# Kernel tuning notes

Hardware: AMD Instinct MI355X
Metric: run time of the kernel (lower is better)

The kernel has to match this reference:

```python
import jax, jax.numpy as jnp
from jax import lax
import numpy as np

T, B, D, H = 2048, 32, 256, 256

def setup_inputs() -> dict:
    key = jax.random.key(0)
    ks = jax.random.split(key, 8)
    inp = {
        'input_': jax.random.normal(ks[0], (T, B, D), dtype=jnp.float32),
        'length': jax.random.randint(ks[1], (B,), 0, T, dtype=jnp.int64),
        'Wih0': jax.random.normal(ks[2], (D, 3 * H), dtype=jnp.float32) * 0.05,
        'Whh0': jax.random.normal(ks[3], (H, 3 * H), dtype=jnp.float32) * 0.05,
        'b0': jax.random.normal(ks[4], (3 * H,), dtype=jnp.float32) * 0.05,
        'Wih1': jax.random.normal(ks[5], (H, 3 * H), dtype=jnp.float32) * 0.05,
        'Whh1': jax.random.normal(ks[6], (H, 3 * H), dtype=jnp.float32) * 0.05,
        'b1': jax.random.normal(ks[7], (3 * H,), dtype=jnp.float32) * 0.05,
    }
    return inp


def _run_layer(x, length, Wih, Whh, b, h0):
    # x: [T, B, D_in]; scan over time with hidden state carried on-chip.
    def step(h, xs):
        x_t, t_idx = xs
        pre = h @ Whh + x_t @ Wih + b          # [B, 3H]
        h_pre, t_pre, _c_pre = jnp.split(pre, 3, axis=1)
        t_gate = jax.nn.sigmoid(t_pre)
        c_gate = jax.nn.sigmoid(t_gate)         # bug-faithful: sigmoid of sigmoid(t_pre)
        s_t = jnp.tanh(h_pre) * t_gate + h * c_gate
        mask = (t_idx < length)[:, None]         # [B, 1]
        h_next = jnp.where(mask, s_t, h)
        return h_next, h_next
    times = jnp.arange(x.shape[0])
    h_n, out = lax.scan(step, h0, (x, times))
    return out, h_n


def reference(input_, length, Wih0, Whh0, b0, Wih1, Whh1, b1):
    h0 = jnp.zeros((input_.shape[1], H), dtype=input_.dtype)
    out0, hn0 = _run_layer(input_, length, Wih0, Whh0, b0, h0)
    # dropout=0 -> identity between layers; each layer reuses the same zero h_0
    out1, hn1 = _run_layer(out0, length, Wih1, Whh1, b1, h0)
    h_n = jnp.stack([hn0, hn1], axis=0)          # [num_layers, B, H]
    return out1, h_n
```

## Files before the change

kernel.cpp:

```cpp
#include <hip/hip_runtime.h>
#include <cstdint>
#include <cstddef>

static constexpr int T_STEPS = 2048;
static constexpr int BATCH   = 32;
static constexpr int DIM     = 256;
static constexpr int NCOL    = 512;
static constexpr size_t M_ROWS = (size_t)T_STEPS * BATCH;

typedef _Float16 f16x4 __attribute__((ext_vector_type(4)));
typedef _Float16 f16x8 __attribute__((ext_vector_type(8)));
typedef float    f32x4 __attribute__((ext_vector_type(4)));
struct alignas(8) H4 { _Float16 x, y, z, w; };

static constexpr size_t XW_OFF   = 0;
static constexpr size_t A_OFF    = M_ROWS * NCOL * 2;
static constexpr size_t BLOB_OFF = A_OFF + M_ROWS * DIM * 2;
static constexpr size_t BLOB_ELT = (size_t)DIM * NCOL;
static constexpr size_t FLAG_OFF = BLOB_OFF + 4 * BLOB_ELT * 2;

__global__ void cvt_f32_to_f16(const float* __restrict__ src, _Float16* __restrict__ dst,
                               int n4, int* __restrict__ flags) {
  if (blockIdx.x == 0 && threadIdx.x < BATCH) flags[threadIdx.x] = 0;
  int i = blockIdx.x * blockDim.x + threadIdx.x;
  if (i >= n4) return;
  float4 v = ((const float4*)src)[i];
  H4 o; o.x = (_Float16)v.x; o.y = (_Float16)v.y; o.z = (_Float16)v.z; o.w = (_Float16)v.w;
  ((H4*)dst)[i] = o;
}

__global__ void prep_blobs4(const float* __restrict__ w0, const float* __restrict__ w1,
                            const float* __restrict__ w2, const float* __restrict__ w3,
                            _Float16* __restrict__ blobs) {
  int gid = blockIdx.x * blockDim.x + threadIdx.x;
  int mat = gid >> 17;
  int rem = gid & 131071;
  int k = rem >> 9;
  int n = rem & 511;
  const float* src = (mat == 0) ? w0 : (mat == 1) ? w1 : (mat == 2) ? w2 : w3;
  float v = src[k * 768 + n];
  int kc = k >> 5, q = (k >> 3) & 3, j = k & 7, tn = n >> 4;
  int lane = (n & 15) + 16 * q;
  blobs[(size_t)mat * BLOB_ELT + ((size_t)(tn * 8 + kc) * 64 + lane) * 8 + j] = (_Float16)v;
}

__global__ __launch_bounds__(256) void gemm_xw(const _Float16* __restrict__ A,
                                               const _Float16* __restrict__ blob,
                                               const float* __restrict__ bias,
                                               _Float16* __restrict__ XW) {
  int lane = threadIdx.x & 63;
  int wave = threadIdx.x >> 6;
  int wid  = blockIdx.x * 4 + wave;
  int mbase = (wid >> 1) * 16;
  int nhalf = wid & 1;
  int q = lane >> 4, n15 = lane & 15;

  f32x4 acc[16];
#pragma unroll
  for (int i = 0; i < 16; i++) acc[i] = (f32x4){0.f, 0.f, 0.f, 0.f};

  const _Float16* Arow = A + (size_t)(mbase + n15) * DIM + q * 8;
#pragma unroll
  for (int kc = 0; kc < 8; kc++) {
    f16x8 af = *(const f16x8*)(Arow + kc * 32);
#pragma unroll
    for (int nt = 0; nt < 16; nt++) {
      const _Float16* bp = blob + ((size_t)((nhalf * 16 + nt) * 8 + kc) * 64 + lane) * 8;
      f16x8 bf = *(const f16x8*)bp;
      acc[nt] = __builtin_amdgcn_mfma_f32_16x16x32_f16(af, bf, acc[nt], 0, 0, 0);
    }
  }
#pragma unroll
  for (int nt = 0; nt < 16; nt++) {
    int col = nhalf * 256 + nt * 16 + n15;
    float bv = bias[col];
#pragma unroll
    for (int r = 0; r < 4; r++) {
      int m = mbase + q * 4 + r;
      XW[(size_t)m * NCOL + col] = (_Float16)(acc[nt][r] + bv);
    }
  }
}

__device__ __forceinline__ int read_len(const void* p, int b) {
  const long long* q = (const long long*)p;
  bool ok64 = true;
  for (int i = 0; i < 32; i++) { long long v = q[i]; if (v < 0 || v > 2048) ok64 = false; }
  return ok64 ? (int)q[b] : ((const int*)p)[b];
}

__device__ __forceinline__ void gload_lds_row(const _Float16* g, _Float16* l) {
  __builtin_amdgcn_global_load_lds(
      (const __attribute__((address_space(1))) void*)g,
      (__attribute__((address_space(3))) void*)l, 16, 0, 0);
}

__device__ __forceinline__ void gate_update(float pre_h, float pre_t, bool live, float& h) {
  const float K1 = 1.442695040888963f, K2 = 2.885390081777927f;
  float phc = fminf(fmaxf(pre_h, -20.f), 20.f);
  float e1 = __builtin_amdgcn_exp2f(-K2 * phc);
  float e2 = __builtin_amdgcn_exp2f(-K1 * pre_t);
  float u1 = 1.f + e1;
  float rr = __builtin_amdgcn_rcpf(u1 * (1.f + e2));
  float ttg = (1.f - e1) * rr;
  float tg  = u1 * rr;
  float cg = 0.5f + tg * (0.250905f + tg * (-0.00432f + tg * (-0.015525f)));
  float s = ttg + h * cg;
  h = live ? s : h;
}

__global__ __launch_bounds__(512, 2) void recur_fused(const _Float16* __restrict__ xw0,
                                                      const _Float16* __restrict__ bwhh0,
                                                      const _Float16* __restrict__ bwhh1,
                                                      const _Float16* __restrict__ bwih1,
                                                      const float* __restrict__ b1,
                                                      const void* __restrict__ lenp,
                                                      _Float16* __restrict__ out0,
                                                      float* __restrict__ out1,
                                                      float* __restrict__ hn,
                                                      int* __restrict__ flags) {
  const int bid  = blockIdx.x;
  const int tid  = threadIdx.x;
  const int w    = tid >> 6;
  const int lane = tid & 63;
  const int q = lane >> 4, l15 = lane & 15;

  __shared__ __align__(16) _Float16 hbuf[2][DIM];
  __shared__ __align__(16) _Float16 xbuf[2][16][NCOL];

  const int c0 = (2 * w) * 16 + l15;
  const int c1 = (2 * w + 1) * 16 + l15;
  constexpr int NB = T_STEPS / 16;

  if (bid < BATCH) {
    const int b = bid;
    const int len = read_len(lenp, b);
    f16x8 Bh[2][8], Bt[2][8];
#pragma unroll
    for (int pp = 0; pp < 2; pp++)
#pragma unroll
      for (int kc = 0; kc < 8; kc++) {
        Bh[pp][kc] = *(const f16x8*)(bwhh0 + ((size_t)((2 * w + pp) * 8 + kc) * 64 + lane) * 8);
        Bt[pp][kc] = *(const f16x8*)(bwhh0 + ((size_t)((16 + 2 * w + pp) * 8 + kc) * 64 + lane) * 8);
      }
    if (tid < DIM) hbuf[0][tid] = (_Float16)0.f;

    const _Float16* xrow = xw0 + (size_t)b * NCOL;
    const size_t xstride = (size_t)BATCH * NCOL;

    gload_lds_row(xrow + (size_t)(2 * w)     * xstride + lane * 8, &xbuf[0][2 * w][0]);
    gload_lds_row(xrow + (size_t)(2 * w + 1) * xstride + lane * 8, &xbuf[0][2 * w + 1][0]);
    asm volatile("s_waitcnt vmcnt(0)" ::: "memory");
    __syncthreads();

    float h0 = 0.f, h1 = 0.f;
    for (int tb = 0; tb < NB; ++tb) {
      const int buf = tb & 1;
      if (tb + 1 < NB) {
        const _Float16* gsrc = xrow + (size_t)((tb + 1) * 16) * xstride;
        gload_lds_row(gsrc + (size_t)(2 * w)     * xstride + lane * 8, &xbuf[1 - buf][2 * w][0]);
        gload_lds_row(gsrc + (size_t)(2 * w + 1) * xstride + lane * 8, &xbuf[1 - buf][2 * w + 1][0]);
      }
#pragma unroll
      for (int ts = 0; ts < 16; ++ts) {
        const int t = tb * 16 + ts;
        const int p = ts & 1;
        const _Float16* xr = &xbuf[buf][ts][0];
        const float xh0 = (float)xr[c0],       xh1 = (float)xr[c1];
        const float xt0 = (float)xr[c0 + 256], xt1 = (float)xr[c1 + 256];

        f32x4 a0 = {0.f, 0.f, 0.f, 0.f}, a1 = a0, a2 = a0, a3 = a0;
        const _Float16* hb = &hbuf[p][q * 8];
#pragma unroll
        for (int kc = 0; kc < 8; kc++) {
          f16x8 a = *(const f16x8*)(hb + kc * 32);
          a0 = __builtin_amdgcn_mfma_f32_16x16x32_f16(a, Bh[0][kc], a0, 0, 0, 0);
          a1 = __builtin_amdgcn_mfma_f32_16x16x32_f16(a, Bh[1][kc], a1, 0, 0, 0);
          a2 = __builtin_amdgcn_mfma_f32_16x16x32_f16(a, Bt[0][kc], a2, 0, 0, 0);
          a3 = __builtin_amdgcn_mfma_f32_16x16x32_f16(a, Bt[1][kc], a3, 0, 0, 0);
        }
        const bool live = t < len;
        gate_update(a0[0] + xh0, a2[0] + xt0, live, h0);
        gate_update(a1[0] + xh1, a3[0] + xt1, live, h1);
        _Float16 s0 = (_Float16)h0, s1 = (_Float16)h1;
        if (q == 0) {
          hbuf[1 - p][c0] = s0;
          hbuf[1 - p][c1] = s1;
          size_t o = ((size_t)t * BATCH + b) * DIM;
          out0[o + c0] = s0; out0[o + c1] = s1;
        }
        if (ts == 15) {
          asm volatile("s_waitcnt vmcnt(0) lgkmcnt(0)\n\ts_barrier" ::: "memory");
        } else {
          asm volatile("s_waitcnt lgkmcnt(0)\n\ts_barrier" ::: "memory");
        }
      }
      if (tid == 0)
        __hip_atomic_store(&flags[b], tb + 1, __ATOMIC_RELEASE, __HIP_MEMORY_SCOPE_AGENT);
    }
    if (q == 0) {
      hn[b * DIM + c0] = h0;
      hn[b * DIM + c1] = h1;
    }
  } else {
    const int b = bid - BATCH;
    const int len = read_len(lenp, b);
    f16x8 Bh[2][8], Bt[2][8];
#pragma unroll
    for (int pp = 0; pp < 2; pp++)
#pragma unroll
      for (int kc = 0; kc < 8; kc++) {
        Bh[pp][kc] = *(const f16x8*)(bwhh1 + ((size_t)((2 * w + pp) * 8 + kc) * 64 + lane) * 8);
        Bt[pp][kc] = *(const f16x8*)(bwhh1 + ((size_t)((16 + 2 * w + pp) * 8 + kc) * 64 + lane) * 8);
      }
    const float bb0 = b1[c0], bb1 = b1[c1], bb2 = b1[c0 + 256], bb3 = b1[c1 + 256];
    if (tid < DIM) hbuf[0][tid] = (_Float16)0.f;
    __syncthreads();

#define WAIT_FLAG(TH_)                                                                   \
    {                                                                                    \
      int it = 0;                                                                        \
      while (__hip_atomic_load(&flags[b], __ATOMIC_RELAXED, __HIP_MEMORY_SCOPE_AGENT)    \
             < (TH_)) {                                                                  \
        __builtin_amdgcn_s_sleep(2);                                                     \
        if (++it > (1 << 22)) break;           \
      }                                                                                  \
      (void)__hip_atomic_load(&flags[b], __ATOMIC_ACQUIRE, __HIP_MEMORY_SCOPE_AGENT);    \
    }

#define XGEMM(XA_, DST_)                                                                 \
    {                                                                                    \
      _Pragma("unroll")                                                                  \
      for (int ti = 0; ti < 4; ti++) {                                                   \
        const int tn = (ti < 2) ? (2 * w + ti) : (16 + 2 * w + (ti - 2));                \
        f32x4 acc = {0.f, 0.f, 0.f, 0.f};                                                \
        _Pragma("unroll")                                                                \
        for (int kc = 0; kc < 8; kc++) {                                                 \
          f16x8 bf = *(const f16x8*)(bwih1 + ((size_t)(tn * 8 + kc) * 64 + lane) * 8);   \
          acc = __builtin_amdgcn_mfma_f32_16x16x32_f16(XA_[kc], bf, acc, 0, 0, 0);       \
        }                                                                                \
        const int   col = (ti == 0) ? c0 : (ti == 1) ? c1 : (ti == 2) ? (c0 + 256)       \
                                                                      : (c1 + 256);      \
        const float bv  = (ti == 0) ? bb0 : (ti == 1) ? bb1 : (ti == 2) ? bb2 : bb3;     \
        _Pragma("unroll")                                                                \
        for (int r = 0; r < 4; r++) xbuf[DST_][q * 4 + r][col] = (_Float16)(acc[r] + bv);\
      }                                                                                  \
    }

    float h0 = 0.f, h1 = 0.f;

    WAIT_FLAG(1);
    {
      const _Float16* arow = out0 + ((size_t)l15 * BATCH + b) * DIM + q * 8;
      f16x8 xa0[8];
#pragma unroll
      for (int kc = 0; kc < 8; kc++) xa0[kc] = *(const f16x8*)(arow + kc * 32);
      XGEMM(xa0, 0);
    }
    asm volatile("s_waitcnt lgkmcnt(0)\n\ts_barrier" ::: "memory");

    f16x8 xa[8];
    for (int tb = 0; tb < NB; ++tb) {
      const int buf = tb & 1;
      if (tb + 1 < NB) {
        WAIT_FLAG(tb + 2);
        const _Float16* arow =
            out0 + ((size_t)((tb + 1) * 16 + l15) * BATCH + b) * DIM + q * 8;
#pragma unroll
        for (int kc = 0; kc < 8; kc++) xa[kc] = *(const f16x8*)(arow + kc * 32);
      }
#pragma unroll
      for (int ts = 0; ts < 16; ++ts) {
        const int t = tb * 16 + ts;
        const int p = ts & 1;
        const _Float16* xr = &xbuf[buf][ts][0];
        const float xh0 = (float)xr[c0],       xh1 = (float)xr[c1];
        const float xt0 = (float)xr[c0 + 256], xt1 = (float)xr[c1 + 256];

        f32x4 a0 = {0.f, 0.f, 0.f, 0.f}, a1 = a0, a2 = a0, a3 = a0;
        const _Float16* hb = &hbuf[p][q * 8];
#pragma unroll
        for (int kc = 0; kc < 8; kc++) {
          f16x8 a = *(const f16x8*)(hb + kc * 32);
          a0 = __builtin_amdgcn_mfma_f32_16x16x32_f16(a, Bh[0][kc], a0, 0, 0, 0);
          a1 = __builtin_amdgcn_mfma_f32_16x16x32_f16(a, Bh[1][kc], a1, 0, 0, 0);
          a2 = __builtin_amdgcn_mfma_f32_16x16x32_f16(a, Bt[0][kc], a2, 0, 0, 0);
          a3 = __builtin_amdgcn_mfma_f32_16x16x32_f16(a, Bt[1][kc], a3, 0, 0, 0);
        }
        const bool live = t < len;
        gate_update(a0[0] + xh0, a2[0] + xt0, live, h0);
        gate_update(a1[0] + xh1, a3[0] + xt1, live, h1);
        if (q == 0) {
          hbuf[1 - p][c0] = (_Float16)h0;
          hbuf[1 - p][c1] = (_Float16)h1;
          size_t o = ((size_t)t * BATCH + b) * DIM;
          out1[o + c0] = h0; out1[o + c1] = h1;
        }
        asm volatile("s_waitcnt lgkmcnt(0)\n\ts_barrier" ::: "memory");
      }
      if (tb + 1 < NB) {
        XGEMM(xa, 1 - buf);
        asm volatile("s_waitcnt lgkmcnt(0)\n\ts_barrier" ::: "memory");
      }
    }
#undef XGEMM
#undef WAIT_FLAG
    if (q == 0) {
      hn[BATCH * DIM + b * DIM + c0] = h0;
      hn[BATCH * DIM + b * DIM + c1] = h1;
    }
  }
}

extern "C" void kernel_launch(void* const* d_in, const int* in_sizes, int n_in,
                              void* d_out, int out_size, void* d_ws, size_t ws_size,
                              hipStream_t stream) {
  const float* input_ = (const float*)d_in[0];
  const void*  lenp   = d_in[1];
  const float* Wih0   = (const float*)d_in[2];
  const float* Whh0   = (const float*)d_in[3];
  const float* b0     = (const float*)d_in[4];
  const float* Wih1   = (const float*)d_in[5];
  const float* Whh1   = (const float*)d_in[6];
  const float* b1     = (const float*)d_in[7];
  float* out = (float*)d_out;
  char*  ws  = (char*)d_ws;

  _Float16* XW    = (_Float16*)(ws + XW_OFF);
  _Float16* Abuf  = (_Float16*)(ws + A_OFF);
  _Float16* blobs = (_Float16*)(ws + BLOB_OFF);
  int*      flags = (int*)(ws + FLAG_OFF);
  float* hn = out + M_ROWS * DIM;

  cvt_f32_to_f16<<<16384, 256, 0, stream>>>(input_, Abuf, (int)(M_ROWS * DIM / 4), flags);
  prep_blobs4<<<2048, 256, 0, stream>>>(Wih0, Wih1, Whh0, Whh1, blobs);
  gemm_xw<<<2048, 256, 0, stream>>>(Abuf, blobs + 0 * BLOB_ELT, b0, XW);
  recur_fused<<<2 * BATCH, 512, 0, stream>>>(XW,
                                             blobs + 2 * BLOB_ELT,
                                             blobs + 3 * BLOB_ELT,
                                             blobs + 1 * BLOB_ELT,
                                             b1, lenp, Abuf, out, hn, flags);
}
```

Baseline: 2.495 ms.

## Move layer-1 input projection into layer-0 blocks via ring buffer

Layer-0 blocks now stage each 16-step block of hidden states in LDS. They compute the layer-1 input GEMM (h·Wih1 + b1) themselves and write the result to a per-batch ring buffer in global memory. Layer-1 blocks then only async-load precomputed projections into LDS, which removes the XGEMM from their serial critical path. A consumer flag adds backpressure so the producer does not overwrite unread ring slots. This moves extra work onto the layer-0 critical path and adds cross-block synchronization overhead.

After: 2.458 ms. No clear change (-1.5%).

```diff
diff --git a/kernel.cpp b/kernel.cpp
--- a/kernel.cpp
+++ b/kernel.cpp
@@ -6,6 +6,7 @@
 static constexpr int BATCH   = 32;
 static constexpr int DIM     = 256;
 static constexpr int NCOL    = 512;
+static constexpr int RB      = 16;
 static constexpr size_t M_ROWS = (size_t)T_STEPS * BATCH;
 
 typedef _Float16 f16x4 __attribute__((ext_vector_type(4)));
@@ -21,7 +22,7 @@
 
 __global__ void cvt_f32_to_f16(const float* __restrict__ src, _Float16* __restrict__ dst,
                                int n4, int* __restrict__ flags) {
-  if (blockIdx.x == 0 && threadIdx.x < BATCH) flags[threadIdx.x] = 0;
+  if (blockIdx.x == 0 && threadIdx.x < 128) flags[threadIdx.x] = 0;
   int i = blockIdx.x * blockDim.x + threadIdx.x;
   if (i >= n4) return;
   float4 v = ((const float4*)src)[i];
@@ -115,7 +116,7 @@
                                                       const _Float16* __restrict__ bwih1,
                                                       const float* __restrict__ b1,
                                                       const void* __restrict__ lenp,
-                                                      _Float16* __restrict__ out0,
+                                                      _Float16* __restrict__ xw1ring,
                                                       float* __restrict__ out1,
                                                       float* __restrict__ hn,
                                                       int* __restrict__ flags) {
@@ -124,9 +125,11 @@
   const int w    = tid >> 6;
   const int lane = tid & 63;
   const int q = lane >> 4, l15 = lane & 15;
+  int* cons_flags = flags + 64;
 
   __shared__ __align__(16) _Float16 hbuf[2][DIM];
   __shared__ __align__(16) _Float16 xbuf[2][16][NCOL];
+  __shared__ __align__(16) _Float16 sbuf[2][16][DIM];
 
   const int c0 = (2 * w) * 16 + l15;
   const int c1 = (2 * w + 1) * 16 + l15;
@@ -143,6 +146,7 @@
         Bh[pp][kc] = *(const f16x8*)(bwhh0 + ((size_t)((2 * w + pp) * 8 + kc) * 64 + lane) * 8);
         Bt[pp][kc] = *(const f16x8*)(bwhh0 + ((size_t)((16 + 2 * w + pp) * 8 + kc) * 64 + lane) * 8);
       }
+    const float bb0 = b1[c0], bb1 = b1[c1], bb2 = b1[c0 + 256], bb3 = b1[c1 + 256];
     if (tid < DIM) hbuf[0][tid] = (_Float16)0.f;
 
     const _Float16* xrow = xw0 + (size_t)b * NCOL;
@@ -154,6 +158,7 @@
     __syncthreads();
 
     float h0 = 0.f, h1 = 0.f;
+    int cons_seen = 0;
     for (int tb = 0; tb < NB; ++tb) {
       const int buf = tb & 1;
       if (tb + 1 < NB) {
@@ -186,8 +191,10 @@
         if (q == 0) {
           hbuf[1 - p][c0] = s0;
           hbuf[1 - p][c1] = s1;
-          size_t o = ((size_t)t * BATCH + b) * DIM;
-          out0[o + c0] = s0; out0[o + c1] = s1;
+          char* sb = (char*)&sbuf[buf][0][0];
+          const int sw = (ts & 7) << 4;
+          *(_Float16*)(sb + ((ts * 512 + c0 * 2) ^ sw)) = s0;
+          *(_Float16*)(sb + ((ts * 512 + c1 * 2) ^ sw)) = s1;
         }
         if (ts == 15) {
           asm volatile("s_waitcnt vmcnt(0) lgkmcnt(0)\n\ts_barrier" ::: "memory");
@@ -195,6 +202,41 @@
           asm volatile("s_waitcnt lgkmcnt(0)\n\ts_barrier" ::: "memory");
         }
       }
+      if (tb - cons_seen >= RB - 2) {
+        int it = 0;
+        while ((cons_seen = __hip_atomic_load(&cons_flags[b], __ATOMIC_RELAXED,
+                                              __HIP_MEMORY_SCOPE_AGENT)) < tb - (RB - 2)) {
+          __builtin_amdgcn_s_sleep(2);
+          if (++it > (1 << 22)) break;
+        }
+      }
+      {
+        const char* sb = (const char*)&sbuf[buf][0][0];
+        f16x8 xa_[8];
+#pragma unroll
+        for (int kc = 0; kc < 8; kc++) {
+          const int off_ = (l15 * 512 + q * 16 + kc * 64) ^ ((l15 & 7) << 4);
+          xa_[kc] = *(const f16x8*)(sb + off_);
+        }
+        _Float16* dst = xw1ring + (size_t)(b * RB + (tb & (RB - 1))) * 16 * NCOL;
+#pragma unroll
+        for (int ti = 0; ti < 4; ti++) {
+          const int tn = (ti < 2) ? (2 * w + ti) : (16 + 2 * w + (ti - 2));
+          f32x4 acc = {0.f, 0.f, 0.f, 0.f};
+#pragma unroll
+          for (int kc = 0; kc < 8; kc++) {
+            f16x8 bf = *(const f16x8*)(bwih1 + ((size_t)(tn * 8 + kc) * 64 + lane) * 8);
+            acc = __builtin_amdgcn_mfma_f32_16x16x32_f16(xa_[kc], bf, acc, 0, 0, 0);
+          }
+          const int   col = (ti == 0) ? c0 : (ti == 1) ? c1 : (ti == 2) ? (c0 + 256)
+                                                                        : (c1 + 256);
+          const float bv  = (ti == 0) ? bb0 : (ti == 1) ? bb1 : (ti == 2) ? bb2 : bb3;
+#pragma unroll
+          for (int r2 = 0; r2 < 4; r2++)
+            dst[(size_t)(q * 4 + r2) * NCOL + col] = (_Float16)(acc[r2] + bv);
+        }
+      }
+      asm volatile("s_waitcnt vmcnt(0) lgkmcnt(0)\n\ts_barrier" ::: "memory");
       if (tid == 0)
         __hip_atomic_store(&flags[b], tb + 1, __ATOMIC_RELEASE, __HIP_MEMORY_SCOPE_AGENT);
     }
@@ -213,7 +255,6 @@
         Bh[pp][kc] = *(const f16x8*)(bwhh1 + ((size_t)((2 * w + pp) * 8 + kc) * 64 + lane) * 8);
         Bt[pp][kc] = *(const f16x8*)(bwhh1 + ((size_t)((16 + 2 * w + pp) * 8 + kc) * 64 + lane) * 8);
       }
-    const float bb0 = b1[c0], bb1 = b1[c1], bb2 = b1[c0 + 256], bb3 = b1[c1 + 256];
     if (tid < DIM) hbuf[0][tid] = (_Float16)0.f;
     __syncthreads();
 
@@ -228,46 +269,26 @@
       (void)__hip_atomic_load(&flags[b], __ATOMIC_ACQUIRE, __HIP_MEMORY_SCOPE_AGENT);    \
     }
 
-#define XGEMM(XA_, DST_)                                                                 \
+#define STAGE_RING(TB_, NB_)                                                             \
     {                                                                                    \
-      _Pragma("unroll")                                                                  \
-      for (int ti = 0; ti < 4; ti++) {                                                   \
-        const int tn = (ti < 2) ? (2 * w + ti) : (16 + 2 * w + (ti - 2));                \
-        f32x4 acc = {0.f, 0.f, 0.f, 0.f};                                                \
-        _Pragma("unroll")                                                                \
-        for (int kc = 0; kc < 8; kc++) {                                                 \
-          f16x8 bf = *(const f16x8*)(bwih1 + ((size_t)(tn * 8 + kc) * 64 + lane) * 8);   \
-          acc = __builtin_amdgcn_mfma_f32_16x16x32_f16(XA_[kc], bf, acc, 0, 0, 0);       \
-        }                                                                                \
-        const int   col = (ti == 0) ? c0 : (ti == 1) ? c1 : (ti == 2) ? (c0 + 256)       \
-                                                                      : (c1 + 256);      \
-        const float bv  = (ti == 0) ? bb0 : (ti == 1) ? bb1 : (ti == 2) ? bb2 : bb3;     \
-        _Pragma("unroll")                                                                \
-        for (int r = 0; r < 4; r++) xbuf[DST_][q * 4 + r][col] = (_Float16)(acc[r] + bv);\
-      }                                                                                  \
+      const _Float16* base =                                                             \
+          xw1ring + (size_t)(b * RB + ((TB_) & (RB - 1))) * 16 * NCOL;                   \
+      gload_lds_row(base + (size_t)(2 * w)     * NCOL + lane * 8, &xbuf[NB_][2 * w][0]); \
+      gload_lds_row(base + (size_t)(2 * w + 1) * NCOL + lane * 8, &xbuf[NB_][2 * w + 1][0]); \
     }
 
     float h0 = 0.f, h1 = 0.f;
 
     WAIT_FLAG(1);
-    {
-      const _Float16* arow = out0 + ((size_t)l15 * BATCH + b) * DIM + q * 8;
-      f16x8 xa0[8];
-#pragma unroll
-      for (int kc = 0; kc < 8; kc++) xa0[kc] = *(const f16x8*)(arow + kc * 32);
-      XGEMM(xa0, 0);
-    }
-    asm volatile("s_waitcnt lgkmcnt(0)\n\ts_barrier" ::: "memory");
-
-    f16x8 xa[8];
+    STAGE_RING(0, 0);
+    asm volatile("s_waitcnt vmcnt(0)" ::: "memory");
+    __syncthreads();
+
     for (int tb = 0; tb < NB; ++tb) {
       const int buf = tb & 1;
       if (tb + 1 < NB) {
         WAIT_FLAG(tb + 2);
-        const _Float16* arow =
-            out0 + ((size_t)((tb + 1) * 16 + l15) * BATCH + b) * DIM + q * 8;
-#pragma unroll
-        for (int kc = 0; kc < 8; kc++) xa[kc] = *(const f16x8*)(arow + kc * 32);
+        STAGE_RING(tb + 1, 1 - buf);
       }
 #pragma unroll
       for (int ts = 0; ts < 16; ++ts) {
@@ -296,14 +317,16 @@
           size_t o = ((size_t)t * BATCH + b) * DIM;
           out1[o + c0] = h0; out1[o + c1] = h1;
         }
-        asm volatile("s_waitcnt lgkmcnt(0)\n\ts_barrier" ::: "memory");
-      }
-      if (tb + 1 < NB) {
-        XGEMM(xa, 1 - buf);
-        asm volatile("s_waitcnt lgkmcnt(0)\n\ts_barrier" ::: "memory");
-      }
-    }
-#undef XGEMM
+        if (ts == 15) {
+          asm volatile("s_waitcnt vmcnt(0) lgkmcnt(0)\n\ts_barrier" ::: "memory");
+        } else {
+          asm volatile("s_waitcnt lgkmcnt(0)\n\ts_barrier" ::: "memory");
+        }
+      }
+      if (((tb & 3) == 3) && tid == 0)
+        __hip_atomic_store(&cons_flags[b], tb + 1, __ATOMIC_RELAXED, __HIP_MEMORY_SCOPE_AGENT);
+    }
+#undef STAGE_RING
 #undef WAIT_FLAG
     if (q == 0) {
       hn[BATCH * DIM + b * DIM + c0] = h0;
@@ -339,5 +362,7 @@
                                              blobs + 2 * BLOB_ELT,
                                              blobs + 3 * BLOB_ELT,
                                              blobs + 1 * BLOB_ELT,
-                                             b1, lenp, Abuf, out, hn, flags);
-}
+                                             b1, lenp,
+                                             Abuf,
+                                             out, hn, flags);
+}
```
